# Kernel tuning notes

Hardware: AMD Instinct MI355X
Metric: run time of the kernel (lower is better)

Reference implementation:

```python
import jax, jax.numpy as jnp
from jax import lax
import numpy as np

B, S, N, F, H = 8, 64, 256, 16, 16
C = N * H  # temporal conv channels = 4096
ALPHA = 0.2
EPS = 1e-5
NEG = -9e15


def setup_inputs() -> dict:
    key = jax.random.key(0)
    ks = jax.random.split(key, 10)
    x = jax.random.normal(ks[0], (B, S, N, F), dtype=jnp.float32)
    adj = jax.random.normal(ks[1], (N, N), dtype=jnp.float32)
    W = jax.random.normal(ks[2], (F, H), dtype=jnp.float32) * (1.414 / np.sqrt(F))
    a = jax.random.normal(ks[3], (2 * H,), dtype=jnp.float32) * (1.414 / np.sqrt(2 * H))
    a1, a2 = a[:H], a[H:]
    conv_w = jax.random.normal(ks[4], (C, C, 3), dtype=jnp.float32) * (1.0 / np.sqrt(C * 3))
    conv_b = jnp.zeros((C,), dtype=jnp.float32)
    bn_gamma = jnp.ones((C,), dtype=jnp.float32)
    bn_beta = jnp.zeros((C,), dtype=jnp.float32)
    bn_mean = jnp.zeros((C,), dtype=jnp.float32)
    bn_var = jnp.ones((C,), dtype=jnp.float32)
    ln_gamma = jnp.ones((H,), dtype=jnp.float32)
    ln_beta = jnp.zeros((H,), dtype=jnp.float32)
    return {"x": x, "adj": adj, "W": W, "a1": a1, "a2": a2,
            "conv_w": conv_w, "conv_b": conv_b,
            "bn_gamma": bn_gamma, "bn_beta": bn_beta,
            "bn_mean": bn_mean, "bn_var": bn_var,
            "ln_gamma": ln_gamma, "ln_beta": ln_beta}


def reference(x, adj, W, a1, a2, conv_w, conv_b, bn_gamma, bn_beta, bn_mean, bn_var, ln_gamma, ln_beta):
    b, s, n, f = x.shape
    h = W.shape[1]
    # --- GAT, batched over all timesteps (eval mode: dropout is identity) ---
    Wh = jnp.einsum('bsnf,fh->bsnh', x, W)            # (B,S,N,H)
    # e_ij = LeakyReLU(a1.Wh_i + a2.Wh_j), equivalent to concat-then-matmul
    f1 = jnp.einsum('bsnh,h->bsn', Wh, a1)
    f2 = jnp.einsum('bsnh,h->bsn', Wh, a2)
    e = jax.nn.leaky_relu(f1[..., :, None] + f2[..., None, :], ALPHA)  # (B,S,N,N)
    e = jnp.where(adj > 0, e, NEG)
    attn = jax.nn.softmax(e, axis=-1)
    spatial = jnp.einsum('bsij,bsjh->bsih', attn, Wh)  # (B,S,N,H)
    # --- temporal conv over seq dim, channels = N*H ---
    t = spatial.reshape(b, s, n * h).transpose(0, 2, 1)  # (B,C,S)
    y = lax.conv_general_dilated(t, conv_w, window_strides=(1,), padding=[(1, 1)],
                                 dimension_numbers=('NCH', 'OIH', 'NCH'))
    y = y + conv_b[None, :, None]
    # BatchNorm1d in eval mode
    y = (y - bn_mean[None, :, None]) / jnp.sqrt(bn_var + EPS)[None, :, None]
    y = y * bn_gamma[None, :, None] + bn_beta[None, :, None]
    y = jax.nn.relu(y)
    temp = y.transpose(0, 2, 1).reshape(b, s, n, h)
    # residual is identity since in_features == hidden_dim
    out = temp + x
    # LayerNorm over last dim
    mu = out.mean(-1, keepdims=True)
    var = out.var(-1, keepdims=True)
    out = (out - mu) / jnp.sqrt(var + EPS) * ln_gamma + ln_beta
    return out
```

## Files before the change

kernel.cpp:

```cpp
#include <hip/hip_runtime.h>
#include <stdint.h>

#define ALPHA 0.2f
#define EPSV  1e-5f

typedef unsigned short u16;
typedef unsigned int   u32;
typedef unsigned long long u64;
typedef __bf16 bf16x8 __attribute__((ext_vector_type(8)));
typedef __bf16 bf16x2 __attribute__((ext_vector_type(2)));
typedef float  f32x4  __attribute__((ext_vector_type(4)));

#define NB 8
#define NS 64
#define NN 256
#define NF 16
#define NH 16
#define NC 4096
#define NK 12288
#define NP 512
#define SROW 66

__device__ __forceinline__ u16 f2b(float f){
  u32 u = __float_as_uint(f);
  u32 r = u + 0x7fffu + ((u>>16)&1u);
  return (u16)(r>>16);
}
__device__ __forceinline__ void un2(u32 v, float& lo, float& hi){
  lo = __uint_as_float(v<<16); hi = __uint_as_float(v & 0xffff0000u);
}
__device__ __forceinline__ void gld16(void* lds, const void* g){
  __builtin_amdgcn_global_load_lds((const __attribute__((address_space(1))) u32*)g,
                                   (__attribute__((address_space(3))) u32*)lds, 16, 0, 0);
}
__device__ __forceinline__ uint4 cvt8(f32x4 a, f32x4 b){
  union { uint4 u; bf16x2 h[4]; } r;
  r.h[0] = (bf16x2){(__bf16)a[0], (__bf16)a[1]};
  r.h[1] = (bf16x2){(__bf16)a[2], (__bf16)a[3]};
  r.h[2] = (bf16x2){(__bf16)b[0], (__bf16)b[1]};
  r.h[3] = (bf16x2){(__bf16)b[2], (__bf16)b[3]};
  return r.u;
}
__device__ __forceinline__ uint2 cvt4(float a, float b, float c, float d){
  union { uint2 u; bf16x2 h[2]; } r;
  r.h[0] = (bf16x2){(__bf16)a, (__bf16)b};
  r.h[1] = (bf16x2){(__bf16)c, (__bf16)d};
  return r.u;
}

__global__ __launch_bounds__(256) void k_adj(const float* __restrict__ adj,
                                             u64* __restrict__ am,
                                             uint4* __restrict__ spz){
  int w = threadIdx.x>>6, l = threadIdx.x&63;
  int row = blockIdx.x*4 + w;
  #pragma unroll
  for(int g=0;g<4;g++){
    float v = adj[(size_t)row*NN + g*64 + l];
    u64 m = __ballot(v > 0.f);
    if(l==0) am[row*4+g] = m;
  }
  if(spz){
    int g = blockIdx.x*256 + threadIdx.x;
    if(g < 8192){
      int r = g>>9;
      int b = r>>1;
      size_t prow = (size_t)b*SROW + ((r&1) ? (SROW-1) : 0);
      spz[prow*512 + (g&511)] = (uint4){0,0,0,0};
    }
  }
}

__global__ __launch_bounds__(256) void k_cw(const float* __restrict__ cw,
                                            u16* __restrict__ Bw){
  int t = threadIdx.x, co = blockIdx.x;
  const float* src = cw + (size_t)co*NK;
  u16* dst = Bw + (size_t)co*NK;
  #pragma unroll
  for(int i=0;i<4;i++){
    int ci0 = (i*256 + t)*4;
    const f32x4* p = (const f32x4*)(src + (size_t)ci0*3);
    f32x4 v0 = p[0];
    f32x4 v1 = p[1];
    f32x4 v2 = p[2];
    uint2 q0 = cvt4(v0[0], v0[3], v1[2], v2[1]);
    uint2 q1 = cvt4(v0[1], v1[0], v1[3], v2[2]);
    uint2 q2 = cvt4(v0[2], v1[1], v2[0], v2[3]);
    *(uint2*)(dst + 0*NC + ci0) = q0;
    *(uint2*)(dst + 1*NC + ci0) = q1;
    *(uint2*)(dst + 2*NC + ci0) = q2;
  }
}

__global__ __launch_bounds__(256) void k_attn(
    const float* __restrict__ x, const float* __restrict__ W,
    const float* __restrict__ a1, const float* __restrict__ a2,
    const u64* __restrict__ am, u16* __restrict__ Sp){
  __shared__ __align__(16) float Ws[NF][NH];
  __shared__ float a1s[NH], a2s[NH];
  __shared__ __align__(16) float Whs[NN][NH];
  __shared__ float f2s[NN];
  int t = threadIdx.x, bs = blockIdx.x;
  int b = bs>>6, s = bs&63;
  Ws[t>>4][t&15] = W[t];
  if(t<NH){ a1s[t]=a1[t]; a2s[t]=a2[t]; }
  u64 mg[4];
  #pragma unroll
  for(int g=0;g<4;g++) mg[g] = am[t*4+g];
  __syncthreads();

  const float* xp = x + ((size_t)bs*NN + t)*NF;
  float xr[16];
  #pragma unroll
  for(int g=0;g<4;g++) *(f32x4*)&xr[g*4] = ((const f32x4*)xp)[g];
  float wh[16];
  #pragma unroll
  for(int h=0;h<16;h++) wh[h]=0.f;
  #pragma unroll
  for(int f=0;f<16;f++){
    float xf = xr[f];
    #pragma unroll
    for(int h=0;h<16;h++) wh[h] = fmaf(xf, Ws[f][h], wh[h]);
  }
  float fi=0.f, s2=0.f;
  #pragma unroll
  for(int h=0;h<16;h++){ fi=fmaf(wh[h],a1s[h],fi); s2=fmaf(wh[h],a2s[h],s2); }
  #pragma unroll
  for(int g=0;g<4;g++) ((f32x4*)Whs[t])[g] = *(f32x4*)&wh[g*4];
  f2s[t] = s2;
  __syncthreads();

  float den = 0.f;
  f32x4 a0={0,0,0,0}, a1v={0,0,0,0}, a2v={0,0,0,0}, a3v={0,0,0,0};
  #pragma unroll
  for(int g=0;g<4;g++){
    u64 mm = mg[g];
    for(int jj=0;jj<64;jj++){
      int j = g*64+jj;
      float e = fi + f2s[j];
      e = e > 0.f ? e : ALPHA*e;
      float p = ((mm>>jj)&1ull) ? __expf(e) : 0.f;
      den += p;
      const f32x4* wr = (const f32x4*)Whs[j];
      a0 += wr[0]*p; a1v += wr[1]*p; a2v += wr[2]*p; a3v += wr[3]*p;
    }
  }
  float inv = 1.f/fmaxf(den, 1e-30f);
  f32x4 o0 = a0*inv, o1 = a1v*inv, o2 = a2v*inv, o3 = a3v*inv;

  uint4 w0 = cvt8(o0,o1), w1 = cvt8(o2,o3);
  uint4* op = (uint4*)(Sp + ((size_t)(b*SROW + s + 1))*NC) + t*2;
  op[0] = w0; op[1] = w1;
}

__global__ __launch_bounds__(256) void k_gemm(
    const u16* __restrict__ Asp, const u16* __restrict__ Bw,
    u16* __restrict__ yp, int kchunk){
  __shared__ __align__(16) u16 As0[128*32];
  __shared__ __align__(16) u16 As1[128*32];
  __shared__ __align__(16) u16 Bs0[128*32];
  __shared__ __align__(16) u16 Bs1[128*32];
  int t = threadIdx.x;
  int id = blockIdx.x;
  int xr_ = id & 7, q0 = id >> 3;
  int mI = q0 & 3, nhi = q0 >> 2;
  int m0 = mI*128, n0 = (nhi*8 + xr_)*128;
  int kbeg = blockIdx.y*kchunk;
  f32x4 acc[4][4];
  #pragma unroll
  for(int i=0;i<4;i++)
    #pragma unroll
    for(int j=0;j<4;j++) acc[i][j] = (f32x4){0,0,0,0};

  int l = t&63, w = t>>6;
  int wm = (w&1)*64, wn = (w>>1)*64;
  int q = l>>4, r16 = l&15;

  int c0 = t, c1 = t+256;
  int mA0 = m0 + (c0>>2), mA1 = m0 + (c1>>2);
  const u16* ga0 = Asp + (size_t)((mA0>>6)*SROW + (mA0&63))*NC + (c0&3)*8;
  const u16* ga1 = Asp + (size_t)((mA1>>6)*SROW + (mA1&63))*NC + (c1&3)*8;
  const u16* gb0 = Bw  + (size_t)(n0 + (c0>>2))*NK + (c0&3)*8;
  const u16* gb1 = Bw  + (size_t)(n0 + (c1>>2))*NK + (c1&3)*8;
  u16 *la00 = As0 + c0*8, *la01 = As0 + c1*8;
  u16 *la10 = As1 + c0*8, *la11 = As1 + c1*8;
  u16 *lb00 = Bs0 + c0*8, *lb01 = Bs0 + c1*8;
  u16 *lb10 = Bs1 + c0*8, *lb11 = Bs1 + c1*8;

  for(int kk=0; kk<kchunk; kk+=64){
    int k0 = kbeg + kk;
    __syncthreads();
    gld16(la00, ga0 + k0);      gld16(la01, ga1 + k0);
    gld16(la10, ga0 + k0 + 32); gld16(la11, ga1 + k0 + 32);
    gld16(lb00, gb0 + k0);      gld16(lb01, gb1 + k0);
    gld16(lb10, gb0 + k0 + 32); gld16(lb11, gb1 + k0 + 32);
    __syncthreads();
    {
      bf16x8 af[4], bfr[4];
      #pragma unroll
      for(int mt=0;mt<4;mt++) af[mt]  = *(const bf16x8*)(As0 + (wm+mt*16+r16)*32 + q*8);
      #pragma unroll
      for(int nt=0;nt<4;nt++) bfr[nt] = *(const bf16x8*)(Bs0 + (wn+nt*16+r16)*32 + q*8);
      #pragma unroll
      for(int mt=0;mt<4;mt++)
        #pragma unroll
        for(int nt=0;nt<4;nt++)
          acc[mt][nt] = __builtin_amdgcn_mfma_f32_16x16x32_bf16(af[mt], bfr[nt], acc[mt][nt], 0,0,0);
    }
    {
      bf16x8 af[4], bfr[4];
      #pragma unroll
      for(int mt=0;mt<4;mt++) af[mt]  = *(const bf16x8*)(As1 + (wm+mt*16+r16)*32 + q*8);
      #pragma unroll
      for(int nt=0;nt<4;nt++) bfr[nt] = *(const bf16x8*)(Bs1 + (wn+nt*16+r16)*32 + q*8);
      #pragma unroll
      for(int mt=0;mt<4;mt++)
        #pragma unroll
        for(int nt=0;nt<4;nt++)
          acc[mt][nt] = __builtin_amdgcn_mfma_f32_16x16x32_bf16(af[mt], bfr[nt], acc[mt][nt], 0,0,0);
    }
  }
  u16* op = yp + (size_t)blockIdx.y*NP*NC;
  #pragma unroll
  for(int mt=0;mt<4;mt++)
    #pragma unroll
    for(int nt=0;nt<4;nt++)
      #pragma unroll
      for(int rr=0;rr<4;rr++){
        int m = m0 + wm + mt*16 + q*4 + rr;
        int n = n0 + wn + nt*16 + r16;
        op[(size_t)m*NC + n] = f2b(acc[mt][nt][rr]);
      }
}

__global__ __launch_bounds__(256) void k_attn_s(
    const float* __restrict__ x, const float* __restrict__ W,
    const float* __restrict__ a1, const float* __restrict__ a2,
    const u64* __restrict__ am, u16* __restrict__ Bt){
  __shared__ __align__(16) float Ws[NF][NH];
  __shared__ float a1s[NH], a2s[NH];
  __shared__ __align__(16) float Whs[NN][NH];
  __shared__ float f2s[NN];
  int t = threadIdx.x, bs = blockIdx.x;
  int b = bs>>6, s = bs&63;
  Ws[t>>4][t&15] = W[t];
  if(t<NH){ a1s[t]=a1[t]; a2s[t]=a2[t]; }
  u64 mg[4];
  #pragma unroll
  for(int g=0;g<4;g++) mg[g] = am[t*4+g];
  __syncthreads();

  const float* xp = x + ((size_t)bs*NN + t)*NF;
  float xr[16];
  #pragma unroll
  for(int g=0;g<4;g++) *(f32x4*)&xr[g*4] = ((const f32x4*)xp)[g];
  float wh[16];
  #pragma unroll
  for(int h=0;h<16;h++) wh[h]=0.f;
  #pragma unroll
  for(int f=0;f<16;f++){
    float xf = xr[f];
    #pragma unroll
    for(int h=0;h<16;h++) wh[h] = fmaf(xf, Ws[f][h], wh[h]);
  }
  float fi=0.f, s2=0.f;
  #pragma unroll
  for(int h=0;h<16;h++){ fi=fmaf(wh[h],a1s[h],fi); s2=fmaf(wh[h],a2s[h],s2); }
  #pragma unroll
  for(int g=0;g<4;g++) ((f32x4*)Whs[t])[g] = *(f32x4*)&wh[g*4];
  f2s[t] = s2;
  __syncthreads();

  float den = 0.f;
  f32x4 a0={0,0,0,0}, a1v={0,0,0,0}, a2v={0,0,0,0}, a3v={0,0,0,0};
  #pragma unroll
  for(int g=0;g<4;g++){
    u64 mm = mg[g];
    for(int jj=0;jj<64;jj++){
      int j = g*64+jj;
      float e = fi + f2s[j];
      e = e > 0.f ? e : ALPHA*e;
      float p = ((mm>>jj)&1ull) ? __expf(e) : 0.f;
      den += p;
      const f32x4* wr = (const f32x4*)Whs[j];
      a0 += wr[0]*p; a1v += wr[1]*p; a2v += wr[2]*p; a3v += wr[3]*p;
    }
  }
  float inv = 1.f/fmaxf(den, 1e-30f);
  float vals[16];
  *(f32x4*)&vals[0]  = a0*inv;  *(f32x4*)&vals[4]  = a1v*inv;
  *(f32x4*)&vals[8]  = a2v*inv; *(f32x4*)&vals[12] = a3v*inv;

  #pragma unroll
  for(int k=0;k<3;k++){
    int cs = s + 1 - k;
    if(cs >= 0 && cs < NS){
      size_t base = ((size_t)(b*NS+cs))*NK + (size_t)t*48 + k;
      #pragma unroll
      for(int h=0;h<16;h++) Bt[base + h*3] = f2b(vals[h]);
    }
  }
  if(s == 0){
    size_t base = ((size_t)(b*NS))*NK + (size_t)t*48;
    #pragma unroll
    for(int h=0;h<16;h++) Bt[base + h*3] = 0;
  }
  if(s == NS-1){
    size_t base = ((size_t)(b*NS+NS-1))*NK + (size_t)t*48 + 2;
    #pragma unroll
    for(int h=0;h<16;h++) Bt[base + h*3] = 0;
  }
}

__global__ __launch_bounds__(256) void k_gemm_f(
    const u16* __restrict__ Abt, const float* __restrict__ Bwf,
    u16* __restrict__ yp, int kchunk){
  __shared__ __align__(16) u16 As0[128*32];
  __shared__ __align__(16) u16 As1[128*32];
  __shared__ __align__(16) u16 Bs0[128*32];
  __shared__ __align__(16) u16 Bs1[128*32];
  int t = threadIdx.x;
  int id = blockIdx.x;
  int xr_ = id & 7, q0 = id >> 3;
  int mI = q0 & 3, nhi = q0 >> 2;
  int m0 = mI*128, n0 = (nhi*8 + xr_)*128;
  int kbeg = blockIdx.y*kchunk;
  f32x4 acc[4][4];
  #pragma unroll
  for(int i=0;i<4;i++)
    #pragma unroll
    for(int j=0;j<4;j++) acc[i][j] = (f32x4){0,0,0,0};

  int l = t&63, w = t>>6;
  int wm = (w&1)*64, wn = (w>>1)*64;
  int q = l>>4, r16 = l&15;

  int c0 = t, c1 = t+256;
  const u16*   ga0 = Abt + (size_t)(m0 + (c0>>2))*NK + (c0&3)*8;
  const u16*   ga1 = Abt + (size_t)(m0 + (c1>>2))*NK + (c1&3)*8;
  const float* gb0 = Bwf + (size_t)(n0 + (c0>>2))*NK + (c0&3)*8;
  const float* gb1 = Bwf + (size_t)(n0 + (c1>>2))*NK + (c1&3)*8;
  u16 *la00 = As0 + c0*8, *la01 = As0 + c1*8;
  u16 *la10 = As1 + c0*8, *la11 = As1 + c1*8;
  u16 *lb00 = Bs0 + c0*8, *lb01 = Bs0 + c1*8;
  u16 *lb10 = Bs1 + c0*8, *lb11 = Bs1 + c1*8;

  for(int kk=0; kk<kchunk; kk+=64){
    int k0 = kbeg + kk;
    f32x4 v00a = *(const f32x4*)(gb0 + k0);
    f32x4 v00b = *(const f32x4*)(gb0 + k0 + 4);
    f32x4 v01a = *(const f32x4*)(gb1 + k0);
    f32x4 v01b = *(const f32x4*)(gb1 + k0 + 4);
    f32x4 v10a = *(const f32x4*)(gb0 + k0 + 32);
    f32x4 v10b = *(const f32x4*)(gb0 + k0 + 36);
    f32x4 v11a = *(const f32x4*)(gb1 + k0 + 32);
    f32x4 v11b = *(const f32x4*)(gb1 + k0 + 36);
    uint4 w00 = cvt8(v00a, v00b);
    uint4 w01 = cvt8(v01a, v01b);
    uint4 w10 = cvt8(v10a, v10b);
    uint4 w11 = cvt8(v11a, v11b);
    __syncthreads();
    gld16(la00, ga0 + k0);      gld16(la01, ga1 + k0);
    gld16(la10, ga0 + k0 + 32); gld16(la11, ga1 + k0 + 32);
    *(uint4*)lb00 = w00; *(uint4*)lb01 = w01;
    *(uint4*)lb10 = w10; *(uint4*)lb11 = w11;
    __syncthreads();
    {
      bf16x8 af[4], bfr[4];
      #pragma unroll
      for(int mt=0;mt<4;mt++) af[mt]  = *(const bf16x8*)(As0 + (wm+mt*16+r16)*32 + q*8);
      #pragma unroll
      for(int nt=0;nt<4;nt++) bfr[nt] = *(const bf16x8*)(Bs0 + (wn+nt*16+r16)*32 + q*8);
      #pragma unroll
      for(int mt=0;mt<4;mt++)
        #pragma unroll
        for(int nt=0;nt<4;nt++)
          acc[mt][nt] = __builtin_amdgcn_mfma_f32_16x16x32_bf16(af[mt], bfr[nt], acc[mt][nt], 0,0,0);
    }
    {
      bf16x8 af[4], bfr[4];
      #pragma unroll
      for(int mt=0;mt<4;mt++) af[mt]  = *(const bf16x8*)(As1 + (wm+mt*16+r16)*32 + q*8);
      #pragma unroll
      for(int nt=0;nt<4;nt++) bfr[nt] = *(const bf16x8*)(Bs1 + (wn+nt*16+r16)*32 + q*8);
      #pragma unroll
      for(int mt=0;mt<4;mt++)
        #pragma unroll
        for(int nt=0;nt<4;nt++)
          acc[mt][nt] = __builtin_amdgcn_mfma_f32_16x16x32_bf16(af[mt], bfr[nt], acc[mt][nt], 0,0,0);
    }
  }
  u16* op = yp + (size_t)blockIdx.y*NP*NC;
  #pragma unroll
  for(int mt=0;mt<4;mt++)
    #pragma unroll
    for(int nt=0;nt<4;nt++)
      #pragma unroll
      for(int rr=0;rr<4;rr++){
        int m = m0 + wm + mt*16 + q*4 + rr;
        int n = n0 + wn + nt*16 + r16;
        op[(size_t)m*NC + n] = f2b(acc[mt][nt][rr]);
      }
}

__global__ __launch_bounds__(256) void k_post(
    const u16* __restrict__ yp, int nparts,
    const float* __restrict__ x,
    const float* __restrict__ cb, const float* __restrict__ bg,
    const float* __restrict__ bb, const float* __restrict__ bm,
    const float* __restrict__ bv, const float* __restrict__ lg,
    const float* __restrict__ lb, float* __restrict__ out){
  int n = threadIdx.x, bs = blockIdx.x;
  float v[16];
  #pragma unroll
  for(int h=0;h<16;h++) v[h]=0.f;
  for(int p=0;p<nparts;p++){
    const u16* pp = yp + (size_t)p*NP*NC + (size_t)bs*NC + n*16;
    uint4 u0 = ((const uint4*)pp)[0];
    uint4 u1 = ((const uint4*)pp)[1];
    float lo, hi;
    un2(u0.x,lo,hi); v[0]+=lo;  v[1]+=hi;
    un2(u0.y,lo,hi); v[2]+=lo;  v[3]+=hi;
    un2(u0.z,lo,hi); v[4]+=lo;  v[5]+=hi;
    un2(u0.w,lo,hi); v[6]+=lo;  v[7]+=hi;
    un2(u1.x,lo,hi); v[8]+=lo;  v[9]+=hi;
    un2(u1.y,lo,hi); v[10]+=lo; v[11]+=hi;
    un2(u1.z,lo,hi); v[12]+=lo; v[13]+=hi;
    un2(u1.w,lo,hi); v[14]+=lo; v[15]+=hi;
  }
  const float* xp = x + ((size_t)bs*NN + n)*NH;
  float xr[16];
  #pragma unroll
  for(int g=0;g<4;g++) *(f32x4*)&xr[g*4] = ((const f32x4*)xp)[g];

  float mu = 0.f;
  #pragma unroll
  for(int h=0;h<16;h++){
    int co = n*16 + h;
    float t1 = v[h] + cb[co];
    t1 = (t1 - bm[co]) * (1.f/sqrtf(bv[co] + EPSV));
    t1 = t1 * bg[co] + bb[co];
    t1 = fmaxf(t1, 0.f);
    t1 += xr[h];
    v[h] = t1; mu += t1;
  }
  mu *= (1.f/16.f);
  float var = 0.f;
  #pragma unroll
  for(int h=0;h<16;h++){ float d = v[h]-mu; var = fmaf(d,d,var); }
  var *= (1.f/16.f);
  float rs = 1.f/sqrtf(var + EPSV);
  float* op = out + ((size_t)bs*NN + n)*NH;
  #pragma unroll
  for(int h=0;h<16;h++) op[h] = (v[h]-mu)*rs*lg[h] + lb[h];
}

extern "C" void kernel_launch(void* const* d_in, const int* in_sizes, int n_in,
                              void* d_out, int out_size, void* d_ws, size_t ws_size,
                              hipStream_t stream){
  const float* x   = (const float*)d_in[0];
  const float* adj = (const float*)d_in[1];
  const float* W   = (const float*)d_in[2];
  const float* a1  = (const float*)d_in[3];
  const float* a2  = (const float*)d_in[4];
  const float* cw  = (const float*)d_in[5];
  const float* cb  = (const float*)d_in[6];
  const float* bg  = (const float*)d_in[7];
  const float* bb  = (const float*)d_in[8];
  const float* bm  = (const float*)d_in[9];
  const float* bv  = (const float*)d_in[10];
  const float* lg  = (const float*)d_in[11];
  const float* lb  = (const float*)d_in[12];
  float* out = (float*)d_out;

  char* ws = (char*)d_ws;
  const size_t ypb = (size_t)NP*NC*2;

  const size_t SP_OFF  = 8192;
  const size_t SP_SZ   = (size_t)NB*SROW*NC*2;
  const size_t BW_OFF  = SP_OFF + SP_SZ;
  const size_t BW_SZ   = (size_t)NC*NK*2;
  const size_t YP_OFF2 = BW_OFF + BW_SZ;

  u64* am = (u64*)ws;

  int P2 = 0;
  if(ws_size >= YP_OFF2 + 8*ypb)      P2 = 8;
  else if(ws_size >= YP_OFF2 + 4*ypb) P2 = 4;
  else if(ws_size >= YP_OFF2 + 2*ypb) P2 = 2;
  else if(ws_size >= YP_OFF2 + 1*ypb) P2 = 1;

  if(P2){
    u16* Sp = (u16*)(ws + SP_OFF);
    u16* Bw = (u16*)(ws + BW_OFF);
    u16* yp = (u16*)(ws + YP_OFF2);
    hipLaunchKernelGGL(k_adj,  dim3(64),      dim3(256), 0, stream, adj, am, (uint4*)Sp);
    hipLaunchKernelGGL(k_cw,   dim3(NC),      dim3(256), 0, stream, cw, Bw);
    hipLaunchKernelGGL(k_attn, dim3(NP),      dim3(256), 0, stream, x,W,a1,a2,am,Sp);
    hipLaunchKernelGGL(k_gemm, dim3(128,P2),  dim3(256), 0, stream, Sp, Bw, yp, NK/P2);
    hipLaunchKernelGGL(k_post, dim3(NP),      dim3(256), 0, stream, yp,P2,x,cb,bg,bb,bm,bv,lg,lb,out);
  } else {
    const size_t BT_OFF = 8192;
    const size_t YP_OFF = BT_OFF + (size_t)NP*NK*2;
    int P = 1;
    if(ws_size >= YP_OFF + 8*ypb)      P = 8;
    else if(ws_size >= YP_OFF + 4*ypb) P = 4;
    else if(ws_size >= YP_OFF + 2*ypb) P = 2;
    u16* Bt = (u16*)(ws + BT_OFF);
    u16* yp = (u16*)(ws + YP_OFF);
    hipLaunchKernelGGL(k_adj,    dim3(64),     dim3(256), 0, stream, adj, am, (uint4*)0);
    hipLaunchKernelGGL(k_attn_s, dim3(NP),     dim3(256), 0, stream, x,W,a1,a2,am,Bt);
    hipLaunchKernelGGL(k_gemm_f, dim3(128,P),  dim3(256), 0, stream, Bt, cw, yp, NK/P);
    hipLaunchKernelGGL(k_post,   dim3(NP),     dim3(256), 0, stream, yp,P,x,cb,bg,bb,bm,bv,lg,lb,out);
  }
}
```

Before: 448.7 us.

## Rework conv GEMM with 256x256 tiles, 4-stage LDS pipeline and swizzle

Replaces the 128x128 double-buffered GEMM with 256x256 block tiles on 512 threads. It uses a 4-buffer global_load_lds prefetch ring with explicit vmcnt waits and a single barrier per K step, plus an XOR swizzle of the LDS layout to avoid bank conflicts. It also adds s_setprio around the MFMA bursts and an XCD-aware block mapping when the split-K factor is 8. The aim is to hide load latency and raise data reuse per block, at the cost of more LDS, higher register pressure (128 accumulators per thread) and fewer blocks in the grid.

```diff
diff --git a/kernel.cpp b/kernel.cpp
--- a/kernel.cpp
+++ b/kernel.cpp
@@ -20,6 +20,7 @@
 #define NK 12288
 #define NP 512
 #define SROW 66
+#define BKT 32
 
 __device__ __forceinline__ u16 f2b(float f){
   u32 u = __float_as_uint(f);
@@ -152,82 +153,118 @@
   op[0] = w0; op[1] = w1;
 }
 
-__global__ __launch_bounds__(256) void k_gemm(
+__global__ __launch_bounds__(512, 2) void k_gemm(
     const u16* __restrict__ Asp, const u16* __restrict__ Bw,
     u16* __restrict__ yp, int kchunk){
-  __shared__ __align__(16) u16 As0[128*32];
-  __shared__ __align__(16) u16 As1[128*32];
-  __shared__ __align__(16) u16 Bs0[128*32];
-  __shared__ __align__(16) u16 Bs1[128*32];
+  __shared__ __align__(16) u16 As[4][256*BKT];
+  __shared__ __align__(16) u16 Bs[4][256*BKT];
   int t = threadIdx.x;
-  int id = blockIdx.x;
-  int xr_ = id & 7, q0 = id >> 3;
-  int mI = q0 & 3, nhi = q0 >> 2;
-  int m0 = mI*128, n0 = (nhi*8 + xr_)*128;
-  int kbeg = blockIdx.y*kchunk;
-  f32x4 acc[4][4];
-  #pragma unroll
-  for(int i=0;i<4;i++)
+
+  int mI, nI, part;
+  if(gridDim.y == 8){
+    int lin = blockIdx.y*32 + blockIdx.x;
+    int xcd = lin & 7, u = lin >> 3;
+    nI = xcd*2 + (u&1); mI = (u>>1)&1; part = u>>2;
+  } else {
+    mI = blockIdx.x & 1; nI = blockIdx.x >> 1; part = blockIdx.y;
+  }
+  int m0 = mI*256, n0 = nI*256;
+  int kbeg = part*kchunk;
+  int NT = kchunk / BKT;
+
+  int c0 = t, c1 = 512 + t;
+  int rA0 = c0>>2, rA1 = c1>>2;
+  int g0 = (c0&3) ^ ((rA0>>1)&3);
+  int g1 = (c1&3) ^ ((rA1>>1)&3);
+  int mr0 = m0 + rA0, mr1 = m0 + rA1;
+  const u16* gaA0 = Asp + (size_t)((mr0>>6)*SROW + (mr0&63))*NC + kbeg + g0*8;
+  const u16* gaA1 = Asp + (size_t)((mr1>>6)*SROW + (mr1&63))*NC + kbeg + g1*8;
+  const u16* gbB0 = Bw  + (size_t)(n0 + rA0)*NK + kbeg + g0*8;
+  const u16* gbB1 = Bw  + (size_t)(n0 + rA1)*NK + kbeg + g1*8;
+  int dA0 = c0*8, dA1 = c1*8;
+
+  int l = t & 63, w = t >> 6;
+  int wr = w >> 2, wc = w & 3;
+  int q = l >> 4, r16 = l & 15;
+
+  int offA[8], offB[4];
+  #pragma unroll
+  for(int mt=0;mt<8;mt++){
+    int row = wr*128 + mt*16 + r16;
+    offA[mt] = row*BKT + ((q ^ ((row>>1)&3))*8);
+  }
+  #pragma unroll
+  for(int nt=0;nt<4;nt++){
+    int row = wc*64 + nt*16 + r16;
+    offB[nt] = row*BKT + ((q ^ ((row>>1)&3))*8);
+  }
+
+  f32x4 acc[8][4];
+  #pragma unroll
+  for(int i=0;i<8;i++)
     #pragma unroll
     for(int j=0;j<4;j++) acc[i][j] = (f32x4){0,0,0,0};
 
-  int l = t&63, w = t>>6;
-  int wm = (w&1)*64, wn = (w>>1)*64;
-  int q = l>>4, r16 = l&15;
-
-  int c0 = t, c1 = t+256;
-  int mA0 = m0 + (c0>>2), mA1 = m0 + (c1>>2);
-  const u16* ga0 = Asp + (size_t)((mA0>>6)*SROW + (mA0&63))*NC + (c0&3)*8;
-  const u16* ga1 = Asp + (size_t)((mA1>>6)*SROW + (mA1&63))*NC + (c1&3)*8;
-  const u16* gb0 = Bw  + (size_t)(n0 + (c0>>2))*NK + (c0&3)*8;
-  const u16* gb1 = Bw  + (size_t)(n0 + (c1>>2))*NK + (c1&3)*8;
-  u16 *la00 = As0 + c0*8, *la01 = As0 + c1*8;
-  u16 *la10 = As1 + c0*8, *la11 = As1 + c1*8;
-  u16 *lb00 = Bs0 + c0*8, *lb01 = Bs0 + c1*8;
-  u16 *lb10 = Bs1 + c0*8, *lb11 = Bs1 + c1*8;
-
-  for(int kk=0; kk<kchunk; kk+=64){
-    int k0 = kbeg + kk;
-    __syncthreads();
-    gld16(la00, ga0 + k0);      gld16(la01, ga1 + k0);
-    gld16(la10, ga0 + k0 + 32); gld16(la11, ga1 + k0 + 32);
-    gld16(lb00, gb0 + k0);      gld16(lb01, gb1 + k0);
-    gld16(lb10, gb0 + k0 + 32); gld16(lb11, gb1 + k0 + 32);
-    __syncthreads();
-    {
-      bf16x8 af[4], bfr[4];
-      #pragma unroll
-      for(int mt=0;mt<4;mt++) af[mt]  = *(const bf16x8*)(As0 + (wm+mt*16+r16)*32 + q*8);
-      #pragma unroll
-      for(int nt=0;nt<4;nt++) bfr[nt] = *(const bf16x8*)(Bs0 + (wn+nt*16+r16)*32 + q*8);
-      #pragma unroll
-      for(int mt=0;mt<4;mt++)
-        #pragma unroll
-        for(int nt=0;nt<4;nt++)
-          acc[mt][nt] = __builtin_amdgcn_mfma_f32_16x16x32_bf16(af[mt], bfr[nt], acc[mt][nt], 0,0,0);
-    }
-    {
-      bf16x8 af[4], bfr[4];
-      #pragma unroll
-      for(int mt=0;mt<4;mt++) af[mt]  = *(const bf16x8*)(As1 + (wm+mt*16+r16)*32 + q*8);
-      #pragma unroll
-      for(int nt=0;nt<4;nt++) bfr[nt] = *(const bf16x8*)(Bs1 + (wn+nt*16+r16)*32 + q*8);
-      #pragma unroll
-      for(int mt=0;mt<4;mt++)
-        #pragma unroll
-        for(int nt=0;nt<4;nt++)
-          acc[mt][nt] = __builtin_amdgcn_mfma_f32_16x16x32_bf16(af[mt], bfr[nt], acc[mt][nt], 0,0,0);
-    }
-  }
-  u16* op = yp + (size_t)blockIdx.y*NP*NC;
-  #pragma unroll
-  for(int mt=0;mt<4;mt++)
+  #pragma unroll
+  for(int Tt=0; Tt<3; ++Tt){
+    size_t ko = (size_t)Tt*BKT;
+    gld16(&As[Tt][dA0], gaA0 + ko); gld16(&As[Tt][dA1], gaA1 + ko);
+    gld16(&Bs[Tt][dA0], gbB0 + ko); gld16(&Bs[Tt][dA1], gbB1 + ko);
+  }
+
+  #define COMPUTE(BUF)                                                        \
+  {                                                                           \
+    const u16* ab = As[(BUF)];                                                \
+    const u16* bb_ = Bs[(BUF)];                                               \
+    bf16x8 af[8], bfr[4];                                                     \
+    _Pragma("unroll")                                                         \
+    for(int mt=0;mt<8;mt++) af[mt] = *(const bf16x8*)(ab + offA[mt]);         \
+    _Pragma("unroll")                                                         \
+    for(int nt=0;nt<4;nt++) bfr[nt] = *(const bf16x8*)(bb_ + offB[nt]);       \
+    __builtin_amdgcn_s_setprio(1);                                            \
+    _Pragma("unroll")                                                         \
+    for(int mt=0;mt<8;mt++)                                                   \
+      _Pragma("unroll")                                                       \
+      for(int nt=0;nt<4;nt++)                                                 \
+        acc[mt][nt] = __builtin_amdgcn_mfma_f32_16x16x32_bf16(                \
+            af[mt], bfr[nt], acc[mt][nt], 0,0,0);                             \
+    __builtin_amdgcn_s_setprio(0);                                            \
+  }
+
+  for(int T=0; T<NT-2; ++T){
+    __builtin_amdgcn_sched_barrier(0);
+    asm volatile("s_waitcnt vmcnt(8)" ::: "memory");
+    __builtin_amdgcn_s_barrier();
+    __builtin_amdgcn_sched_barrier(0);
+    if(T+3 < NT){
+      int b3 = (T+3)&3;
+      size_t ko = (size_t)(T+3)*BKT;
+      gld16(&As[b3][dA0], gaA0 + ko); gld16(&As[b3][dA1], gaA1 + ko);
+      gld16(&Bs[b3][dA0], gbB0 + ko); gld16(&Bs[b3][dA1], gbB1 + ko);
+    }
+    COMPUTE(T&3);
+  }
+  __builtin_amdgcn_sched_barrier(0);
+  asm volatile("s_waitcnt vmcnt(4)" ::: "memory");
+  __builtin_amdgcn_s_barrier();
+  __builtin_amdgcn_sched_barrier(0);
+  COMPUTE((NT-2)&3);
+  __builtin_amdgcn_sched_barrier(0);
+  asm volatile("s_waitcnt vmcnt(0)" ::: "memory");
+  __builtin_amdgcn_s_barrier();
+  __builtin_amdgcn_sched_barrier(0);
+  COMPUTE((NT-1)&3);
+  #undef COMPUTE
+
+  u16* op = yp + (size_t)part*NP*NC;
+  #pragma unroll
+  for(int mt=0;mt<8;mt++)
     #pragma unroll
     for(int nt=0;nt<4;nt++)
       #pragma unroll
       for(int rr=0;rr<4;rr++){
-        int m = m0 + wm + mt*16 + q*4 + rr;
-        int n = n0 + wn + nt*16 + r16;
+        int m = m0 + wr*128 + mt*16 + q*4 + rr;
+        int n = n0 + wc*64 + nt*16 + r16;
         op[(size_t)m*NC + n] = f2b(acc[mt][nt][rr]);
       }
 }
@@ -496,7 +533,7 @@
     hipLaunchKernelGGL(k_adj,  dim3(64),      dim3(256), 0, stream, adj, am, (uint4*)Sp);
     hipLaunchKernelGGL(k_cw,   dim3(NC),      dim3(256), 0, stream, cw, Bw);
     hipLaunchKernelGGL(k_attn, dim3(NP),      dim3(256), 0, stream, x,W,a1,a2,am,Sp);
-    hipLaunchKernelGGL(k_gemm, dim3(128,P2),  dim3(256), 0, stream, Sp, Bw, yp, NK/P2);
+    hipLaunchKernelGGL(k_gemm, dim3(32,P2),   dim3(512), 0, stream, Sp, Bw, yp, NK/P2);
     hipLaunchKernelGGL(k_post, dim3(NP),      dim3(256), 0, stream, yp,P2,x,cb,bg,bb,bm,bv,lg,lb,out);
   } else {
     const size_t BT_OFF = 8192;
```

New measurement: 444.2 us. No clear change (-1.0%).
